# Kernel optimization log

Hardware: AMD Instinct MI355X
Metric: run time of the kernel (lower is better)

## Reference

```python
import jax, jax.numpy as jnp
import numpy as np

C = 256          # hidden_channels
H = 8            # num_heads
NP = 512         # (poly_order+1)**3 nodes per element
NFULL = 65536    # num_elements * NP
NRED = 50000     # reduced (deduplicated) node count
MAX_WAVELENGTH = 100


def layernorm(x, w, b, eps=1e-5):
    m = x.mean(-1, keepdims=True)
    v = ((x - m) ** 2).mean(-1, keepdims=True)
    return (x - m) / jnp.sqrt(v + eps) * w + b


def apply_rope(x, coords, max_wavelength=MAX_WAVELENGTH):
    # x: (ne, h, np, c), coords: (ne, np, 3). Output feature dim = 3*per_dim_features (may truncate).
    n_dim = coords.shape[-1]
    feat = x.shape[-1]
    pdf = 2 * (feat // (2 * n_dim))   # per-dim rotated features
    half = pdf // 2
    fraction = 2.0 * jnp.arange(half, dtype=x.dtype) / pdf
    timescale = max_wavelength ** fraction  # (half,)
    chunks = []
    for i in range(n_dim):
        xc = x[..., i * pdf:(i + 1) * pdf]                 # (ne,h,np,pdf)
        theta = coords[..., i][..., None] / timescale       # (ne,np,half)
        sin = jnp.sin(theta)[:, None, :, :]                 # (ne,1,np,half)
        cos = jnp.cos(theta)[:, None, :, :]
        f, s = xc[..., :half], xc[..., half:]
        chunks.append(jnp.concatenate([f * cos - s * sin, s * cos + f * sin], axis=-1))
    return jnp.concatenate(chunks, axis=-1).astype(x.dtype)


def setup_inputs() -> dict:
    key = jax.random.key(0)
    ks = jax.random.split(key, 12)
    s = 0.06  # ~xavier scale for 256-dim linears
    return {
        "x": jax.random.normal(ks[0], (NRED, C), dtype=jnp.float32),
        "pos": jax.random.uniform(ks[1], (NRED, 3), dtype=jnp.float32),
        "index": jax.random.randint(ks[2], (NRED,), 0, NRED),
        "idx_reduced2full": jax.random.randint(ks[3], (NFULL,), 0, NRED),
        "idx_full2reduced": jax.random.randint(ks[4], (NRED,), 0, NFULL),
        "norm1_w": jnp.ones((C,), jnp.float32),
        "norm1_b": jnp.zeros((C,), jnp.float32),
        "q_w": jax.random.normal(ks[5], (C, C), dtype=jnp.float32) * s,
        "k_w": jax.random.normal(ks[6], (C, C), dtype=jnp.float32) * s,
        "v_w": jax.random.normal(ks[7], (C, C), dtype=jnp.float32) * s,
        "o_w": jax.random.normal(ks[8], (C, C), dtype=jnp.float32) * s,
        "norm2_w": jnp.ones((C,), jnp.float32),
        "norm2_b": jnp.zeros((C,), jnp.float32),
        "ffn_w1": jax.random.normal(ks[9], (2 * C, C), dtype=jnp.float32) * s,
        "ffn_w2": jax.random.normal(ks[10], (C, C), dtype=jnp.float32) * s,
    }


def reference(x, pos, index, idx_reduced2full, idx_full2reduced,
              norm1_w, norm1_b, q_w, k_w, v_w, o_w,
              norm2_w, norm2_b, ffn_w1, ffn_w2):
    ne = idx_reduced2full.shape[0] // NP
    c = x.shape[-1]
    # gather reduced nodes into per-element blocks
    xf = x[idx_reduced2full].reshape(ne, NP, c)
    pf = pos[idx_reduced2full].reshape(ne, NP, 3)
    min_pos = jnp.array([-10.0, -1.0, 0.0], dtype=pf.dtype)
    max_pos = jnp.array([25.0, 5.0, 2.0], dtype=pf.dtype)
    pf = (pf - min_pos) / (max_pos - min_pos)
    xn = layernorm(xf, norm1_w, norm1_b)
    # torch Linear: y = x @ W.T
    def proj(t, w):
        y = jnp.einsum('eni,oi->eno', t, w)
        return y.reshape(ne, NP, H, c // H).transpose(0, 2, 1, 3)  # (ne,h,np,hd)
    q = apply_rope(proj(xn, q_w), pf)   # (ne,h,np,30) -- RoPE truncates head dim
    k = apply_rope(proj(xn, k_w), pf)
    v = proj(xn, v_w)                   # (ne,h,np,32)
    scale = 1.0 / jnp.sqrt(jnp.asarray(q.shape[-1], q.dtype))  # sdpa scales by post-rope q dim
    scores = jnp.einsum('ehqc,ehkc->ehqk', q, k) * scale
    attn = jax.nn.softmax(scores, axis=-1)
    out = jnp.einsum('ehqk,ehkc->ehqc', attn, v)
    out = out.transpose(0, 2, 1, 3).reshape(ne, NP, c)
    out = jnp.einsum('eni,oi->eno', out, o_w).reshape(ne * NP, c)
    # scatter_mean over duplicated (shared) nodes, keyed by original node index
    seg = index[idx_reduced2full]
    sums = jax.ops.segment_sum(out, seg, num_segments=NRED)
    cnts = jax.ops.segment_sum(jnp.ones((ne * NP,), out.dtype), seg, num_segments=NRED)
    mean = sums / jnp.maximum(cnts, 1.0)[:, None]
    ao = mean[seg][idx_full2reduced]    # back to reduced ordering, (NRED, c)
    x2 = x + ao                          # SIZE == 1 path
    y = layernorm(x2, norm2_w, norm2_b)
    h = jnp.einsum('ni,oi->no', y, ffn_w1)
    a, g = jnp.split(h, 2, axis=-1)
    y = jnp.einsum('ni,oi->no', a * jax.nn.silu(g), ffn_w2)
    return x2 + y
```

## Files before the change

### kernel.cpp

```cpp
#include <hip/hip_runtime.h>
#include <hip/hip_bf16.h>
#include <cstddef>

#define C_DIM 256
#define HEADS 8
#define HD 32
#define NPTS 512
#define NFULL_N 65536
#define NRED_N 50000
#define NE_N 128

typedef __attribute__((ext_vector_type(8))) short short8;
typedef __attribute__((ext_vector_type(4))) float floatx4;
typedef __attribute__((ext_vector_type(4))) unsigned uintx4;

__device__ __forceinline__ float wave_reduce_sum(float v) {
#pragma unroll
  for (int off = 1; off < 64; off <<= 1) v += __shfl_xor(v, off, 64);
  return v;
}

__device__ __forceinline__ unsigned short f2bf(float f) {
  union { float f; unsigned u; } x; x.f = f;
  unsigned r = x.u + 0x7FFF + ((x.u >> 16) & 1);
  return (unsigned short)(r >> 16);
}

__device__ __forceinline__ float bf2f(unsigned short u) {
  union { unsigned u; float f; } x; x.u = ((unsigned)u) << 16;
  return x.f;
}

__device__ __forceinline__ float fast_exp2(float x) {
#if __has_builtin(__builtin_amdgcn_exp2f)
  return __builtin_amdgcn_exp2f(x);
#else
  return exp2f(x);
#endif
}

__device__ __forceinline__ float fast_rcp(float x) {
#if __has_builtin(__builtin_amdgcn_rcpf)
  return __builtin_amdgcn_rcpf(x);
#else
  return 1.0f / x;
#endif
}

__device__ __forceinline__ int xcd_logical(int bid, int nwg) {
  int q = nwg >> 3, r = nwg & 7;
  int xcd = bid & 7, s = bid >> 3;
  int base = (xcd < r) ? xcd * (q + 1) : r * (q + 1) + (xcd - r) * q;
  return base + s;
}

__global__ __launch_bounds__(256) void cvt_all_kernel(
    const float* __restrict__ qw, const float* __restrict__ kw,
    const float* __restrict__ vw, const float* __restrict__ ow,
    const float* __restrict__ w1, const float* __restrict__ w2,
    unsigned short* __restrict__ qwb, unsigned short* __restrict__ kwb,
    unsigned short* __restrict__ vwb, unsigned short* __restrict__ owb,
    unsigned short* __restrict__ w1b, unsigned short* __restrict__ w2b)
{
  int i = blockIdx.x * 256 + threadIdx.x;
  const float* src; unsigned short* dst; int o;
  if      (i <  16384) { src = qw; dst = qwb; o = i; }
  else if (i <  32768) { src = kw; dst = kwb; o = i - 16384; }
  else if (i <  49152) { src = vw; dst = vwb; o = i - 32768; }
  else if (i <  65536) { src = ow; dst = owb; o = i - 49152; }
  else if (i <  98304) { src = w1; dst = w1b; o = i - 65536; }
  else                 { src = w2; dst = w2b; o = i - 98304; }
  float4 v = *(const float4*)&src[o << 2];
  unsigned u0 = f2bf(v.x) | ((unsigned)f2bf(v.y) << 16);
  unsigned u1 = f2bf(v.z) | ((unsigned)f2bf(v.w) << 16);
  *(uint2*)&dst[o << 2] = make_uint2(u0, u1);
}

__global__ __launch_bounds__(256) void ln_kernel(
    const float* __restrict__ x, const int* __restrict__ gidx,
    const float* __restrict__ w, const float* __restrict__ b,
    unsigned short* __restrict__ out, int nrows,
    const int* __restrict__ index, float* __restrict__ cnts)
{
  int wave = threadIdx.x >> 6, lane = threadIdx.x & 63;
  int row = blockIdx.x * 4 + wave;
  if (row >= nrows) return;
  int src = gidx ? gidx[row] : row;
  if (cnts && lane == 0) atomicAdd(&cnts[index[src]], 1.0f);
  const float* xr = x + (size_t)src * C_DIM;
  float4 v = *(const float4*)&xr[lane << 2];
  float s  = v.x + v.y + v.z + v.w;
  float sq = v.x*v.x + v.y*v.y + v.z*v.z + v.w*v.w;
  s  = wave_reduce_sum(s);
  sq = wave_reduce_sum(sq);
  float mean = s * (1.0f / 256.0f);
  float var  = sq * (1.0f / 256.0f) - mean * mean;
  float rstd = rsqrtf(var + 1e-5f);
  float4 wv = *(const float4*)&w[lane << 2];
  float4 bv = *(const float4*)&b[lane << 2];
  float ox = (v.x - mean) * rstd * wv.x + bv.x;
  float oy = (v.y - mean) * rstd * wv.y + bv.y;
  float oz = (v.z - mean) * rstd * wv.z + bv.z;
  float ow = (v.w - mean) * rstd * wv.w + bv.w;
  unsigned u0 = f2bf(ox) | ((unsigned)f2bf(oy) << 16);
  unsigned u1 = f2bf(oz) | ((unsigned)f2bf(ow) << 16);
  *(uint2*)&out[(size_t)row * C_DIM + (lane << 2)] = make_uint2(u0, u1);
}

__global__ __launch_bounds__(256) void qkv_kernel(
    const unsigned short* __restrict__ A,
    const unsigned short* __restrict__ Bq, const unsigned short* __restrict__ Bk,
    const unsigned short* __restrict__ Bv,
    unsigned short* __restrict__ qo, unsigned short* __restrict__ ko,
    unsigned short* __restrict__ vo)
{
  __shared__ unsigned short As[128 * 32];
  __shared__ unsigned short Bqs[64 * 32];
  __shared__ unsigned short Bks[64 * 32];
  __shared__ unsigned short Bvs[64 * 32];
  const int tid = threadIdx.x;
  const int lane = tid & 63, w = tid >> 6;
  const int wr = w >> 1, wc = w & 1;
  const int l15 = lane & 15, g = lane >> 4;
  const int L = xcd_logical(blockIdx.x, 2048);
  const int bn = L & 3;
  const int bm = (L >> 2) * 128;
  floatx4 acc[3][4][2] = {};
  const int sr = lane >> 2;
  const int sk = (lane & 3) << 3;
  for (int k0 = 0; k0 < 256; k0 += 32) {
#pragma unroll
    for (int c = 0; c < 2; ++c) {
      int stripe = w * 2 + c;
      const unsigned short* ga = A + (size_t)(bm + stripe * 16 + sr) * 256 + k0 + sk;
      __builtin_amdgcn_global_load_lds(
          (const __attribute__((address_space(1))) void*)ga,
          (__attribute__((address_space(3))) void*)&As[stripe * 512], 16, 0, 0);
    }
#pragma unroll
    for (int c = 0; c < 3; ++c) {
      int idx = w * 3 + c;
      int t = idx >> 2, rs = idx & 3;
      const unsigned short* Bt = (t == 0) ? Bq : (t == 1) ? Bk : Bv;
      unsigned short* ldst = (t == 0) ? &Bqs[rs * 512]
                           : (t == 1) ? &Bks[rs * 512] : &Bvs[rs * 512];
      const unsigned short* gsrc = Bt + (size_t)(bn * 64 + rs * 16 + sr) * 256 + k0 + sk;
      __builtin_amdgcn_global_load_lds(
          (const __attribute__((address_space(1))) void*)gsrc,
          (__attribute__((address_space(3))) void*)ldst, 16, 0, 0);
    }
    __syncthreads();
    const int arow = wr * 64 + l15;
    const int brow = wc * 32 + l15;
    const int kb = g << 3;
    short8 af[4], bq[2], bk[2], bv[2];
#pragma unroll
    for (int m = 0; m < 4; ++m)
      af[m] = *(const short8*)&As[(arow + m * 16) * 32 + kb];
#pragma unroll
    for (int n = 0; n < 2; ++n) {
      bq[n] = *(const short8*)&Bqs[(brow + n * 16) * 32 + kb];
      bk[n] = *(const short8*)&Bks[(brow + n * 16) * 32 + kb];
      bv[n] = *(const short8*)&Bvs[(brow + n * 16) * 32 + kb];
    }
#pragma unroll
    for (int m = 0; m < 4; ++m)
#pragma unroll
      for (int n = 0; n < 2; ++n) {
        acc[0][m][n] = __builtin_amdgcn_mfma_f32_16x16x32_bf16(af[m], bq[n], acc[0][m][n], 0, 0, 0);
        acc[1][m][n] = __builtin_amdgcn_mfma_f32_16x16x32_bf16(af[m], bk[n], acc[1][m][n], 0, 0, 0);
        acc[2][m][n] = __builtin_amdgcn_mfma_f32_16x16x32_bf16(af[m], bv[n], acc[2][m][n], 0, 0, 0);
      }
    __syncthreads();
  }
  const int cgrp = bn * 2 + wc;
  const int crow0 = bm + wr * 64 + (g << 2);
#pragma unroll
  for (int m = 0; m < 4; ++m) {
#pragma unroll
    for (int j = 0; j < 4; ++j) {
      int row = crow0 + m * 16 + j;
      size_t hb = ((size_t)((row >> 9) * 8 + cgrp) * 512 + (row & 511)) * 32;
#pragma unroll
      for (int n = 0; n < 2; ++n) {
        int cc = n * 16 + l15;
        qo[hb + cc] = f2bf(acc[0][m][n][j]);
        ko[hb + cc] = f2bf(acc[1][m][n][j]);
        vo[hb + cc] = f2bf(acc[2][m][n][j]);
      }
    }
  }
}

__global__ __launch_bounds__(256) void gemm_bf16(
    const unsigned short* __restrict__ A, const unsigned short* __restrict__ B,
    void* __restrict__ Cv, const float* __restrict__ res,
    const int* __restrict__ seg_index, const int* __restrict__ seg_r2f,
    int M, int N, int K, int mode)
{
  __shared__ unsigned short As[64 * 32];
  __shared__ unsigned short Bs[128 * 32];
  const int tid = threadIdx.x;
  const int lane = tid & 63, w = tid >> 6;
  const int l15 = lane & 15, g = lane >> 4;
  const int L = xcd_logical(blockIdx.x, gridDim.x);
  const int bn = (L & 1) * 128;
  const int bm = (L >> 1) * 64;
  floatx4 acc[4][2] = {};
  const int sr = (lane >> 2);
  const int sk = (lane & 3) << 3;
  for (int k0 = 0; k0 < K; k0 += 32) {
    {
      const unsigned short* ga = A + (size_t)(bm + w * 16 + sr) * K + k0 + sk;
      __builtin_amdgcn_global_load_lds(
          (const __attribute__((address_space(1))) void*)ga,
          (__attribute__((address_space(3))) void*)&As[w * 512], 16, 0, 0);
    }
#pragma unroll
    for (int c = 0; c < 2; ++c) {
      int stripe = w * 2 + c;
      const unsigned short* gb = B + (size_t)(bn + stripe * 16 + sr) * K + k0 + sk;
      __builtin_amdgcn_global_load_lds(
          (const __attribute__((address_space(1))) void*)gb,
          (__attribute__((address_space(3))) void*)&Bs[stripe * 512], 16, 0, 0);
    }
    __syncthreads();
    const int kb = g << 3;
    short8 af[4], bfr[2];
#pragma unroll
    for (int m = 0; m < 4; ++m)
      af[m] = *(const short8*)&As[(m * 16 + l15) * 32 + kb];
#pragma unroll
    for (int n = 0; n < 2; ++n)
      bfr[n] = *(const short8*)&Bs[(w * 32 + n * 16 + l15) * 32 + kb];
#pragma unroll
    for (int m = 0; m < 4; ++m)
#pragma unroll
      for (int n = 0; n < 2; ++n)
        acc[m][n] = __builtin_amdgcn_mfma_f32_16x16x32_bf16(
            af[m], bfr[n], acc[m][n], 0, 0, 0);
    __syncthreads();
  }
  const int crow0 = bm + (g << 2);
  const int ccol0 = bn + w * 32 + l15;
#pragma unroll
  for (int m = 0; m < 4; ++m) {
#pragma unroll
    for (int j = 0; j < 4; ++j) {
      int row = crow0 + m * 16 + j;
      if (row >= M) continue;
      if (mode == 0) {
        float* C = (float*)Cv;
        size_t off = (size_t)row * N + ccol0;
#pragma unroll
        for (int n = 0; n < 2; ++n) {
          float v = acc[m][n][j];
          if (res) v += res[off + n * 16];
          C[off + n * 16] = v;
        }
      } else if (mode == 3) {
        unsigned short* C = (unsigned short*)Cv;
        size_t off = (size_t)row * N + ccol0;
#pragma unroll
        for (int n = 0; n < 2; ++n) C[off + n * 16] = f2bf(acc[m][n][j]);
      } else {
        unsigned short* S = (unsigned short*)Cv;
        int s = seg_index[seg_r2f[row]];
        int gbase = lane & 48;
        int le = (2 * l15) & 15;
        int lo = (2 * l15 + 1) & 15;
        bool hi = (l15 >= 8);
        float va = acc[m][0][j];
        float vb = acc[m][1][j];
        float ae = __shfl(va, gbase + le, 64);
        float be = __shfl(vb, gbase + le, 64);
        float ao = __shfl(va, gbase + lo, 64);
        float bo = __shfl(vb, gbase + lo, 64);
        float ev = hi ? be : ae;
        float ov = hi ? bo : ao;
        unsigned pair = (unsigned)f2bf(ev) | ((unsigned)f2bf(ov) << 16);
        unsigned short* addr =
            S + (size_t)s * N + (bn + w * 32) + 2 * l15;
        asm volatile("global_atomic_pk_add_bf16 %0, %1, off"
                     :: "v"(addr), "v"(pair) : "memory");
      }
    }
  }
  if (mode == 4) asm volatile("s_waitcnt vmcnt(0)");
}

__global__ __launch_bounds__(256) void rope_qk_kernel(
    unsigned short* __restrict__ qb, unsigned short* __restrict__ kb,
    const float* __restrict__ pos, const int* __restrict__ r2f, float qscale)
{
  int row = blockIdx.x * 256 + threadIdx.x;
  if (row >= NFULL_N * HEADS) return;
  int e = row >> 12, p = row & 511;
  int j = (e << 9) | p;
  int pi = r2f[j];
  float pf[3];
  pf[0] = (pos[pi * 3 + 0] + 10.0f) * (1.0f / 35.0f);
  pf[1] = (pos[pi * 3 + 1] + 1.0f)  * (1.0f / 6.0f);
  pf[2] =  pos[pi * 3 + 2] * 0.5f;
  const float invts[5] = {1.0f, 0.3981071706f, 0.1584893192f,
                          0.0630957344f, 0.0251188643f};
  float sn[15], cs[15];
#pragma unroll
  for (int i = 0; i < 3; ++i)
#pragma unroll
    for (int t = 0; t < 5; ++t) {
      float theta = pf[i] * invts[t];
      sn[i * 5 + t] = sinf(theta);
      cs[i * 5 + t] = cosf(theta);
    }
  unsigned short* qr = qb + (size_t)row * 32;
  unsigned short* kr = kb + (size_t)row * 32;
  uint4 qraw[4], kraw[4];
#pragma unroll
  for (int u = 0; u < 4; ++u) { qraw[u] = *(const uint4*)&qr[u * 8];
                                kraw[u] = *(const uint4*)&kr[u * 8]; }
  float q[32], k[32];
  const unsigned short* qs = (const unsigned short*)qraw;
  const unsigned short* ks = (const unsigned short*)kraw;
#pragma unroll
  for (int d = 0; d < 32; ++d) { q[d] = bf2f(qs[d]); k[d] = bf2f(ks[d]); }
#pragma unroll
  for (int i = 0; i < 3; ++i)
#pragma unroll
    for (int t = 0; t < 5; ++t) {
      int fo = i * 10 + t, so = fo + 5, ti = i * 5 + t;
      float c0 = cs[ti], s0 = sn[ti];
      float qf = q[fo], qq = q[so];
      q[fo] = qf * c0 - qq * s0;
      q[so] = qq * c0 + qf * s0;
      float kf = k[fo], kk = k[so];
      k[fo] = kf * c0 - kk * s0;
      k[so] = kk * c0 + kf * s0;
    }
  q[30] = 0.f; q[31] = 0.f; k[30] = 0.f; k[31] = 0.f;
  unsigned qo[16], ko[16];
#pragma unroll
  for (int u = 0; u < 16; ++u) {
    qo[u] = f2bf(q[2*u] * qscale) | ((unsigned)f2bf(q[2*u+1] * qscale) << 16);
    ko[u] = f2bf(k[2*u]) | ((unsigned)f2bf(k[2*u+1]) << 16);
  }
#pragma unroll
  for (int u = 0; u < 4; ++u) {
    *(uint4*)&qr[u * 8] = make_uint4(qo[4*u], qo[4*u+1], qo[4*u+2], qo[4*u+3]);
    *(uint4*)&kr[u * 8] = make_uint4(ko[4*u], ko[4*u+1], ko[4*u+2], ko[4*u+3]);
  }
}

__global__ __launch_bounds__(512, 4) void attn_mfma_kernel(
    const unsigned short* __restrict__ qh, const unsigned short* __restrict__ kh,
    const unsigned short* __restrict__ vh, unsigned short* __restrict__ ob)
{
  __shared__ unsigned short K_lds[256 * 40];
  __shared__ unsigned short V_lds[32 * 264];
  const int blk = blockIdx.x;
  const int e = blk >> 3, head = blk & 7;
  const int tid = threadIdx.x;
  const int w = tid >> 6, lane = tid & 63;
  const int l15 = lane & 15, g = lane >> 4;
  const size_t rowbase = (size_t)blk * 512;

  short8 qfrag[4];
#pragma unroll
  for (int qt = 0; qt < 4; ++qt) {
    size_t qrow = rowbase + w * 64 + qt * 16 + l15;
    qfrag[qt] = *(const short8*)&qh[qrow * 32 + g * 8];
  }
  floatx4 oacc[4][2] = {};
  floatx4 accl[4] = {};
  const short one_bf = (short)0x3F80;
  const short8 ones8 = {one_bf, one_bf, one_bf, one_bf,
                        one_bf, one_bf, one_bf, one_bf};
  const float C2 = 28.853900817779268f;
  const floatx4 mc2 = {-C2, -C2, -C2, -C2};

  for (int stage = 0; stage < 2; ++stage) {
    const int kc0 = stage * 256;
    __syncthreads();
    {
      const unsigned short* khp = kh + (rowbase + kc0) * 32;
      int r = tid >> 1, half = tid & 1;
      uint4 a = *(const uint4*)&khp[(size_t)r * 32 + half * 16];
      uint4 b = *(const uint4*)&khp[(size_t)r * 32 + half * 16 + 8];
      *(uint4*)&K_lds[r * 40 + half * 16]     = a;
      *(uint4*)&K_lds[r * 40 + half * 16 + 8] = b;
    }
    {
      int key = tid >> 1, dq = tid & 1;
      const unsigned short* vrow = vh + (rowbase + kc0 + key) * 32 + dq * 16;
      unsigned short tmp[16];
      *(uint4*)&tmp[0] = *(const uint4*)vrow;
      *(uint4*)&tmp[8] = *(const uint4*)(vrow + 8);
      int lam = key & 31;
      int pc = ((lam & 15) >> 2) * 8 + (lam & 3) + ((lam >> 4) << 2);
      int ccol = (key & ~31) + pc;
#pragma unroll
      for (int d = 0; d < 16; ++d)
        V_lds[(dq * 16 + d) * 264 + ccol] = tmp[d];
    }
    __syncthreads();
    for (int c = 0; c < 8; ++c) {
      short8 kf0 = *(const short8*)&K_lds[(c * 32 + l15) * 40 + g * 8];
      short8 kf1 = *(const short8*)&K_lds[(c * 32 + 16 + l15) * 40 + g * 8];
      short8 vf0 = *(const short8*)&V_lds[l15 * 264 + c * 32 + g * 8];
      short8 vf1 = *(const short8*)&V_lds[(16 + l15) * 264 + c * 32 + g * 8];
      __builtin_amdgcn_s_setprio(1);
#pragma unroll
      for (int qt = 0; qt < 4; ++qt) {
        floatx4 s0 = __builtin_amdgcn_mfma_f32_16x16x32_bf16(kf0, qfrag[qt], mc2, 0, 0, 0);
        floatx4 s1 = __builtin_amdgcn_mfma_f32_16x16x32_bf16(kf1, qfrag[qt], mc2, 0, 0, 0);
        float p0 = fast_exp2(s0[0]), p1 = fast_exp2(s0[1]);
        float p2 = fast_exp2(s0[2]), p3 = fast_exp2(s0[3]);
        float p4 = fast_exp2(s1[0]), p5 = fast_exp2(s1[1]);
        float p6 = fast_exp2(s1[2]), p7 = fast_exp2(s1[3]);
        uintx4 uv = {
          __builtin_amdgcn_perm(__builtin_bit_cast(unsigned, p1),
                                __builtin_bit_cast(unsigned, p0), 0x07060302u),
          __builtin_amdgcn_perm(__builtin_bit_cast(unsigned, p3),
                                __builtin_bit_cast(unsigned, p2), 0x07060302u),
          __builtin_amdgcn_perm(__builtin_bit_cast(unsigned, p5),
                                __builtin_bit_cast(unsigned, p4), 0x07060302u),
          __builtin_amdgcn_perm(__builtin_bit_cast(unsigned, p7),
                                __builtin_bit_cast(unsigned, p6), 0x07060302u)};
        short8 ps8 = __builtin_bit_cast(short8, uv);
        oacc[qt][0] = __builtin_amdgcn_mfma_f32_16x16x32_bf16(ps8, vf0, oacc[qt][0], 0, 0, 0);
        oacc[qt][1] = __builtin_amdgcn_mfma_f32_16x16x32_bf16(ps8, vf1, oacc[qt][1], 0, 0, 0);
        accl[qt]    = __builtin_amdgcn_mfma_f32_16x16x32_bf16(ps8, ones8, accl[qt], 0, 0, 0);
      }
      __builtin_amdgcn_s_setprio(0);
    }
  }
  const size_t obase = ((size_t)e * 512) * 256 + head * 32;
#pragma unroll
  for (int qt = 0; qt < 4; ++qt) {
#pragma unroll
    for (int j = 0; j < 4; ++j) {
      float inv = fast_rcp(accl[qt][j]);
      int p = w * 64 + qt * 16 + g * 4 + j;
      size_t off = obase + (size_t)p * 256 + l15;
      ob[off]      = f2bf(oacc[qt][0][j] * inv);
      ob[off + 16] = f2bf(oacc[qt][1][j] * inv);
    }
  }
}

__global__ __launch_bounds__(256) void addmean_ln2_kernel(
    const float* __restrict__ x, const int* __restrict__ index,
    const int* __restrict__ r2f, const int* __restrict__ f2r,
    const unsigned short* __restrict__ sums, const float* __restrict__ cnts,
    const float* __restrict__ w, const float* __restrict__ b,
    float* __restrict__ x2, unsigned short* __restrict__ ln2b)
{
  int wave = threadIdx.x >> 6, lane = threadIdx.x & 63;
  int r = blockIdx.x * 4 + wave;
  if (r >= NRED_N) return;
  int j = f2r[r];
  int s = index[r2f[j]];
  float inv = 1.0f / fmaxf(cnts[s], 1.0f);
  uint2 sr = *(const uint2*)&sums[(size_t)s * C_DIM + (lane << 2)];
  float4 sv = make_float4(bf2f((unsigned short)(sr.x & 0xFFFF)),
                          bf2f((unsigned short)(sr.x >> 16)),
                          bf2f((unsigned short)(sr.y & 0xFFFF)),
                          bf2f((unsigned short)(sr.y >> 16)));
  float4 xv = *(const float4*)&x[(size_t)r * C_DIM + (lane << 2)];
  float4 o = make_float4(xv.x + sv.x * inv, xv.y + sv.y * inv,
                         xv.z + sv.z * inv, xv.w + sv.w * inv);
  *(float4*)&x2[(size_t)r * C_DIM + (lane << 2)] = o;
  float ssum = o.x + o.y + o.z + o.w;
  float sq = o.x*o.x + o.y*o.y + o.z*o.z + o.w*o.w;
  ssum = wave_reduce_sum(ssum);
  sq   = wave_reduce_sum(sq);
  float mean = ssum * (1.0f / 256.0f);
  float var  = sq * (1.0f / 256.0f) - mean * mean;
  float rstd = rsqrtf(var + 1e-5f);
  float4 wv = *(const float4*)&w[lane << 2];
  float4 bv = *(const float4*)&b[lane << 2];
  float ox = (o.x - mean) * rstd * wv.x + bv.x;
  float oy = (o.y - mean) * rstd * wv.y + bv.y;
  float oz = (o.z - mean) * rstd * wv.z + bv.z;
  float ow = (o.w - mean) * rstd * wv.w + bv.w;
  unsigned u0 = f2bf(ox) | ((unsigned)f2bf(oy) << 16);
  unsigned u1 = f2bf(oz) | ((unsigned)f2bf(ow) << 16);
  *(uint2*)&ln2b[(size_t)r * C_DIM + (lane << 2)] = make_uint2(u0, u1);
}

__global__ __launch_bounds__(256) void ffn1_act_kernel(
    const unsigned short* __restrict__ A, const unsigned short* __restrict__ B,
    unsigned short* __restrict__ act, int M)
{
  __shared__ unsigned short As[64 * 32];
  __shared__ unsigned short Bas[128 * 32];
  __shared__ unsigned short Bgs[128 * 32];
  const int tid = threadIdx.x;
  const int lane = tid & 63, w = tid >> 6;
  const int l15 = lane & 15, g = lane >> 4;
  const int L = xcd_logical(blockIdx.x, gridDim.x);
  const int bn = L & 1;
  const int bm = (L >> 1) * 64;
  floatx4 acc_a[4][2] = {}, acc_g[4][2] = {};
  const int sr = (lane >> 2);
  const int sk = (lane & 3) << 3;
  for (int k0 = 0; k0 < 256; k0 += 32) {
    {
      const unsigned short* ga = A + (size_t)(bm + w * 16 + sr) * 256 + k0 + sk;
      __builtin_amdgcn_global_load_lds(
          (const __attribute__((address_space(1))) void*)ga,
          (__attribute__((address_space(3))) void*)&As[w * 512], 16, 0, 0);
    }
#pragma unroll
    for (int c = 0; c < 2; ++c) {
      int stripe = w * 2 + c;
      const unsigned short* gba = B + (size_t)(bn * 128 + stripe * 16 + sr) * 256 + k0 + sk;
      const unsigned short* gbg = B + (size_t)(256 + bn * 128 + stripe * 16 + sr) * 256 + k0 + sk;
      __builtin_amdgcn_global_load_lds(
          (const __attribute__((address_space(1))) void*)gba,
          (__attribute__((address_space(3))) void*)&Bas[stripe * 512], 16, 0, 0);
      __builtin_amdgcn_global_load_lds(
          (const __attribute__((address_space(1))) void*)gbg,
          (__attribute__((address_space(3))) void*)&Bgs[stripe * 512], 16, 0, 0);
    }
    __syncthreads();
    const int kb = g << 3;
    short8 af[4], ba[2], bg2[2];
#pragma unroll
    for (int m = 0; m < 4; ++m)
      af[m] = *(const short8*)&As[(m * 16 + l15) * 32 + kb];
#pragma unroll
    for (int n = 0; n < 2; ++n) {
      ba[n]  = *(const short8*)&Bas[(w * 32 + n * 16 + l15) * 32 + kb];
      bg2[n] = *(const short8*)&Bgs[(w * 32 + n * 16 + l15) * 32 + kb];
    }
#pragma unroll
    for (int m = 0; m < 4; ++m)
#pragma unroll
      for (int n = 0; n < 2; ++n) {
        acc_a[m][n] = __builtin_amdgcn_mfma_f32_16x16x32_bf16(
            af[m], ba[n], acc_a[m][n], 0, 0, 0);
        acc_g[m][n] = __builtin_amdgcn_mfma_f32_16x16x32_bf16(
            af[m], bg2[n], acc_g[m][n], 0, 0, 0);
      }
    __syncthreads();
  }
  const int crow0 = bm + (g << 2);
  const int ccol0 = bn * 128 + w * 32 + l15;
  const float LOG2E = 1.4426950408889634f;
#pragma unroll
  for (int m = 0; m < 4; ++m) {
#pragma unroll
    for (int j = 0; j < 4; ++j) {
      int row = crow0 + m * 16 + j;
      if (row >= M) continue;
      size_t off = (size_t)row * 256 + ccol0;
#pragma unroll
      for (int n = 0; n < 2; ++n) {
        float a = acc_a[m][n][j];
        float gg = acc_g[m][n][j];
        float eneg = fast_exp2(-gg * LOG2E);
        float v = a * gg * fast_rcp(1.0f + eneg);
        act[off + n * 16] = f2bf(v);
      }
    }
  }
}

extern "C" void kernel_launch(void* const* d_in, const int* in_sizes, int n_in,
                              void* d_out, int out_size, void* d_ws, size_t ws_size,
                              hipStream_t stream)
{
  const float* x    = (const float*)d_in[0];
  const float* pos  = (const float*)d_in[1];
  const int*   index= (const int*)d_in[2];
  const int*   r2f  = (const int*)d_in[3];
  const int*   f2r  = (const int*)d_in[4];
  const float* n1w  = (const float*)d_in[5];
  const float* n1b  = (const float*)d_in[6];
  const float* qw   = (const float*)d_in[7];
  const float* kw   = (const float*)d_in[8];
  const float* vw   = (const float*)d_in[9];
  const float* ow   = (const float*)d_in[10];
  const float* n2w  = (const float*)d_in[11];
  const float* n2b  = (const float*)d_in[12];
  const float* w1   = (const float*)d_in[13];
  const float* w2   = (const float*)d_in[14];
  float* out = (float*)d_out;

  char* ws = (char*)d_ws;
  unsigned short* xnbf = (unsigned short*)(ws);
  unsigned short* qhh  = (unsigned short*)(ws + 33554432);
  unsigned short* khh  = (unsigned short*)(ws + 67108864);
  unsigned short* vhh  = (unsigned short*)(ws + 100663296);
  float* x2   = (float*)(ws + 134217728);
  float* cnts = (float*)(ws + 185417728);
  unsigned short* wbf = (unsigned short*)(ws + 185617728);
  unsigned short* sums = (unsigned short*)(ws + 186646528);
  unsigned short* qwb = wbf;
  unsigned short* kwb = wbf + 65536;
  unsigned short* vwb = wbf + 2 * 65536;
  unsigned short* owb = wbf + 3 * 65536;
  unsigned short* w1b = wbf + 4 * 65536;
  unsigned short* w2b = wbf + 6 * 65536;
  unsigned short* attn_out = xnbf;
  unsigned short* ln2b = xnbf;
  unsigned short* actb = qhh;

  hipMemsetAsync(sums, 0, (size_t)NRED_N * C_DIM * 2, stream);
  hipMemsetAsync(cnts, 0, (size_t)NRED_N * 4, stream);
  cvt_all_kernel<<<448, 256, 0, stream>>>(qw, kw, vw, ow, w1, w2,
                                          qwb, kwb, vwb, owb, w1b, w2b);
  ln_kernel<<<NFULL_N / 4, 256, 0, stream>>>(x, r2f, n1w, n1b, xnbf, NFULL_N,
                                             index, cnts);
  qkv_kernel<<<2048, 256, 0, stream>>>(xnbf, qwb, kwb, vwb, qhh, khh, vhh);
  const float C1 = 0.26339891f;
  rope_qk_kernel<<<NFULL_N * HEADS / 256, 256, 0, stream>>>(qhh, khh, pos, r2f, C1);
  attn_mfma_kernel<<<NE_N * HEADS, 512, 0, stream>>>(qhh, khh, vhh, attn_out);
  gemm_bf16<<<2048, 256, 0, stream>>>(attn_out, owb, sums, nullptr,
                                      index, r2f, NFULL_N, C_DIM, C_DIM, 4);
  addmean_ln2_kernel<<<(NRED_N + 3) / 4, 256, 0, stream>>>(
      x, index, r2f, f2r, sums, cnts, n2w, n2b, x2, ln2b);
  ffn1_act_kernel<<<1564, 256, 0, stream>>>(ln2b, w1b, actb, NRED_N);
  gemm_bf16<<<1564, 256, 0, stream>>>(actb, w2b, out, x2,
                                      nullptr, nullptr, NRED_N, C_DIM, C_DIM, 0);
}
```

Before: 312.6 us.

## Fuse RoPE and q scaling into QKV projection epilogue via LDS transpose

```diff
diff --git a/kernel.cpp b/kernel.cpp
--- a/kernel.cpp
+++ b/kernel.cpp
@@ -111,13 +111,15 @@
     const unsigned short* __restrict__ A,
     const unsigned short* __restrict__ Bq, const unsigned short* __restrict__ Bk,
     const unsigned short* __restrict__ Bv,
+    const float* __restrict__ pos, const int* __restrict__ r2f,
     unsigned short* __restrict__ qo, unsigned short* __restrict__ ko,
-    unsigned short* __restrict__ vo)
+    unsigned short* __restrict__ vo, float qscale)
 {
   __shared__ unsigned short As[128 * 32];
   __shared__ unsigned short Bqs[64 * 32];
   __shared__ unsigned short Bks[64 * 32];
   __shared__ unsigned short Bvs[64 * 32];
+  __shared__ unsigned short Tile[128 * 64];
   const int tid = threadIdx.x;
   const int lane = tid & 63, w = tid >> 6;
   const int wr = w >> 1, wc = w & 1;
@@ -173,22 +175,78 @@
       }
     __syncthreads();
   }
-  const int cgrp = bn * 2 + wc;
+  const int cgrp0 = bn * 2 + wc;
   const int crow0 = bm + wr * 64 + (g << 2);
 #pragma unroll
   for (int m = 0; m < 4; ++m) {
 #pragma unroll
     for (int j = 0; j < 4; ++j) {
       int row = crow0 + m * 16 + j;
-      size_t hb = ((size_t)((row >> 9) * 8 + cgrp) * 512 + (row & 511)) * 32;
-#pragma unroll
-      for (int n = 0; n < 2; ++n) {
-        int cc = n * 16 + l15;
-        qo[hb + cc] = f2bf(acc[0][m][n][j]);
-        ko[hb + cc] = f2bf(acc[1][m][n][j]);
-        vo[hb + cc] = f2bf(acc[2][m][n][j]);
+      size_t hb = ((size_t)((row >> 9) * 8 + cgrp0) * 512 + (row & 511)) * 32;
+#pragma unroll
+      for (int n = 0; n < 2; ++n)
+        vo[hb + n * 16 + l15] = f2bf(acc[2][m][n][j]);
+    }
+  }
+  const int rr = tid & 127;
+  const int half = tid >> 7;
+  const int jrow = bm + rr;
+  const int pi = r2f[jrow];
+  float pf[3];
+  pf[0] = (pos[pi * 3 + 0] + 10.0f) * (1.0f / 35.0f);
+  pf[1] = (pos[pi * 3 + 1] + 1.0f)  * (1.0f / 6.0f);
+  pf[2] =  pos[pi * 3 + 2] * 0.5f;
+  const size_t hbw = ((size_t)((jrow >> 9) * 8 + bn * 2 + half) * 512 +
+                      (jrow & 511)) * 32;
+  const int rst = wr * 64 + (g << 2);
+  const float invts[5] = {1.0f, 0.3981071706f, 0.1584893192f,
+                          0.0630957344f, 0.0251188643f};
+#pragma unroll
+  for (int tq = 0; tq < 2; ++tq) {
+    __syncthreads();
+#pragma unroll
+    for (int m = 0; m < 4; ++m)
+#pragma unroll
+      for (int j = 0; j < 4; ++j) {
+        int r0 = rst + m * 16 + j;
+#pragma unroll
+        for (int n = 0; n < 2; ++n) {
+          int idx = r0 * 64 + wc * 32 + n * 16 + l15;
+          Tile[idx ^ ((r0 & 7) << 3)] = f2bf(acc[tq][m][n][j]);
+        }
       }
-    }
+    __syncthreads();
+    float qv[32];
+    int base = rr * 64 + half * 32;
+    int swz = (rr & 7) << 3;
+#pragma unroll
+    for (int u = 0; u < 4; ++u) {
+      uint4 raw = *(const uint4*)&Tile[(base + u * 8) ^ swz];
+      const unsigned short* rs2 = (const unsigned short*)&raw;
+#pragma unroll
+      for (int d = 0; d < 8; ++d) qv[u * 8 + d] = bf2f(rs2[d]);
+    }
+#pragma unroll
+    for (int i = 0; i < 3; ++i)
+#pragma unroll
+      for (int t5 = 0; t5 < 5; ++t5) {
+        float theta = pf[i] * invts[t5];
+        float sn = sinf(theta), cst = cosf(theta);
+        int fo = i * 10 + t5, so = fo + 5;
+        float a = qv[fo], b2 = qv[so];
+        qv[fo] = a * cst - b2 * sn;
+        qv[so] = b2 * cst + a * sn;
+      }
+    qv[30] = 0.f; qv[31] = 0.f;
+    float scl = (tq == 0) ? qscale : 1.0f;
+    unsigned po[16];
+#pragma unroll
+    for (int u = 0; u < 16; ++u)
+      po[u] = f2bf(qv[2*u] * scl) | ((unsigned)f2bf(qv[2*u+1] * scl) << 16);
+    unsigned short* dst = (tq == 0 ? qo : ko) + hbw;
+#pragma unroll
+    for (int u = 0; u < 4; ++u)
+      *(uint4*)&dst[u * 8] = make_uint4(po[4*u], po[4*u+1], po[4*u+2], po[4*u+3]);
   }
 }
 
@@ -287,68 +345,6 @@
     }
   }
   if (mode == 4) asm volatile("s_waitcnt vmcnt(0)");
-}
-
-__global__ __launch_bounds__(256) void rope_qk_kernel(
-    unsigned short* __restrict__ qb, unsigned short* __restrict__ kb,
-    const float* __restrict__ pos, const int* __restrict__ r2f, float qscale)
-{
-  int row = blockIdx.x * 256 + threadIdx.x;
-  if (row >= NFULL_N * HEADS) return;
-  int e = row >> 12, p = row & 511;
-  int j = (e << 9) | p;
-  int pi = r2f[j];
-  float pf[3];
-  pf[0] = (pos[pi * 3 + 0] + 10.0f) * (1.0f / 35.0f);
-  pf[1] = (pos[pi * 3 + 1] + 1.0f)  * (1.0f / 6.0f);
-  pf[2] =  pos[pi * 3 + 2] * 0.5f;
-  const float invts[5] = {1.0f, 0.3981071706f, 0.1584893192f,
-                          0.0630957344f, 0.0251188643f};
-  float sn[15], cs[15];
-#pragma unroll
-  for (int i = 0; i < 3; ++i)
-#pragma unroll
-    for (int t = 0; t < 5; ++t) {
-      float theta = pf[i] * invts[t];
-      sn[i * 5 + t] = sinf(theta);
-      cs[i * 5 + t] = cosf(theta);
-    }
-  unsigned short* qr = qb + (size_t)row * 32;
-  unsigned short* kr = kb + (size_t)row * 32;
-  uint4 qraw[4], kraw[4];
-#pragma unroll
-  for (int u = 0; u < 4; ++u) { qraw[u] = *(const uint4*)&qr[u * 8];
-                                kraw[u] = *(const uint4*)&kr[u * 8]; }
-  float q[32], k[32];
-  const unsigned short* qs = (const unsigned short*)qraw;
-  const unsigned short* ks = (const unsigned short*)kraw;
-#pragma unroll
-  for (int d = 0; d < 32; ++d) { q[d] = bf2f(qs[d]); k[d] = bf2f(ks[d]); }
-#pragma unroll
-  for (int i = 0; i < 3; ++i)
-#pragma unroll
-    for (int t = 0; t < 5; ++t) {
-      int fo = i * 10 + t, so = fo + 5, ti = i * 5 + t;
-      float c0 = cs[ti], s0 = sn[ti];
-      float qf = q[fo], qq = q[so];
-      q[fo] = qf * c0 - qq * s0;
-      q[so] = qq * c0 + qf * s0;
-      float kf = k[fo], kk = k[so];
-      k[fo] = kf * c0 - kk * s0;
-      k[so] = kk * c0 + kf * s0;
-    }
-  q[30] = 0.f; q[31] = 0.f; k[30] = 0.f; k[31] = 0.f;
-  unsigned qo[16], ko[16];
-#pragma unroll
-  for (int u = 0; u < 16; ++u) {
-    qo[u] = f2bf(q[2*u] * qscale) | ((unsigned)f2bf(q[2*u+1] * qscale) << 16);
-    ko[u] = f2bf(k[2*u]) | ((unsigned)f2bf(k[2*u+1]) << 16);
-  }
-#pragma unroll
-  for (int u = 0; u < 4; ++u) {
-    *(uint4*)&qr[u * 8] = make_uint4(qo[4*u], qo[4*u+1], qo[4*u+2], qo[4*u+3]);
-    *(uint4*)&kr[u * 8] = make_uint4(ko[4*u], ko[4*u+1], ko[4*u+2], ko[4*u+3]);
-  }
 }
 
 __global__ __launch_bounds__(512, 4) void attn_mfma_kernel(
@@ -613,9 +609,9 @@
                                           qwb, kwb, vwb, owb, w1b, w2b);
   ln_kernel<<<NFULL_N / 4, 256, 0, stream>>>(x, r2f, n1w, n1b, xnbf, NFULL_N,
                                              index, cnts);
-  qkv_kernel<<<2048, 256, 0, stream>>>(xnbf, qwb, kwb, vwb, qhh, khh, vhh);
   const float C1 = 0.26339891f;
-  rope_qk_kernel<<<NFULL_N * HEADS / 256, 256, 0, stream>>>(qhh, khh, pos, r2f, C1);
+  qkv_kernel<<<2048, 256, 0, stream>>>(xnbf, qwb, kwb, vwb, pos, r2f,
+                                       qhh, khh, vhh, C1);
   attn_mfma_kernel<<<NE_N * HEADS, 512, 0, stream>>>(qhh, khh, vhh, attn_out);
   gemm_bf16<<<2048, 256, 0, stream>>>(attn_out, owb, sums, nullptr,
                                       index, r2f, NFULL_N, C_DIM, C_DIM, 4);
```

Result: slower. 341.9 us (+9.4%).
